# Kernel tuning notes

Hardware: AMD Instinct MI355X
Metric: run time of the kernel (lower is better)

The kernel has to match this reference:

```python
import jax, jax.numpy as jnp
import numpy as np

WINDOW_SIZE = 128
NEG = -1e9

def setup_inputs() -> dict:
    key = jax.random.key(0)
    kq, kk, kv = jax.random.split(key, 3)
    B, H, T, D = 2, 16, 2048, 64
    q = jax.random.normal(kq, (B, H, T, D), dtype=jnp.float32)
    k = jax.random.normal(kk, (B, H, T, D), dtype=jnp.float32)
    v = jax.random.normal(kv, (B, H, T, D), dtype=jnp.float32)
    return {"q": q, "k": k, "v": v}

def reference(q, k, v):
    # q,k,v: (B, H, T, D)
    D = q.shape[-1]
    Tq, Tk = q.shape[2], k.shape[2]
    scale = 1.0 / jnp.sqrt(jnp.asarray(D, dtype=q.dtype))
    scores = jnp.einsum('bhqd,bhkd->bhqk', q, k) * scale  # (B,H,Tq,Tk)
    dist = jnp.abs(jnp.arange(Tq)[:, None] - jnp.arange(Tk)[None, :])
    window_mask = dist <= WINDOW_SIZE  # (Tq,Tk)
    scores = jnp.where(window_mask[None, None], scores, jnp.asarray(NEG, dtype=scores.dtype))
    attn = jax.nn.softmax(scores, axis=-1)
    output = jnp.einsum('bhqk,bhkd->bhqd', attn, v)
    return (output, attn)
```

## Files before the change

kernel.cpp:

```cpp
#include <hip/hip_runtime.h>
#include <hip/hip_bf16.h>

typedef short bf16x8 __attribute__((ext_vector_type(8)));
typedef float f32x4 __attribute__((ext_vector_type(4)));

#define T_DIM 2048
#define D_DIM 64
#define WIN 128
#define QBLK 64
#define NEGBIG -1e30f
#define NZE 116

__device__ __forceinline__ short f2b(float x) {
  __hip_bfloat16 h = __float2bfloat16(x);
  return *reinterpret_cast<short*>(&h);
}
__device__ __forceinline__ float b2f(short s) {
  unsigned u = ((unsigned)(unsigned short)s) << 16;
  return __builtin_bit_cast(float, u);
}
__device__ __forceinline__ bf16x8 cvt8(f32x4 a, f32x4 b) {
  bf16x8 r;
  r[0] = f2b(a[0]); r[1] = f2b(a[1]); r[2] = f2b(a[2]); r[3] = f2b(a[3]);
  r[4] = f2b(b[0]); r[5] = f2b(b[1]); r[6] = f2b(b[2]); r[7] = f2b(b[3]);
  return r;
}
__device__ __forceinline__ int swzV(int row, int b) { return row * 640 + (b ^ ((row & 7) << 4)); }

#define ZEMIT(n) do { \
  for (int _i = 0; _i < (n); ++_i) { \
    if (zt < NZE) { \
      const int zr = (tid >> 3) + 32 * (zt & 1); \
      const int zc = (tid & 7) + 8 * (zt >> 1); \
      if (zc < rowg) { \
        const int c4 = zc << 2; \
        const int col = (c4 < Lw) ? c4 : (kend + c4 - Lw); \
        __builtin_nontemporal_store(zvec, (f32x4*)(azero + (size_t)zr * T_DIM + col)); \
      } \
      ++zt; \
    } \
  } } while (0)

__global__ __launch_bounds__(256, 3) void lsa_one(
    const float* __restrict__ Qg, const float* __restrict__ Kg,
    const float* __restrict__ Vg, float* __restrict__ Og,
    float* __restrict__ Ag) {
  const int tid = threadIdx.x;
  const int work = ((blockIdx.x & 7) << 7) + (blockIdx.x >> 3);
  const int bh = work >> 5;
  const int qb = work & 31;
  const int q0 = qb * QBLK;
  int kstart = q0 - WIN; if (kstart < 0) kstart = 0;
  int kend = q0 + QBLK + WIN; if (kend > T_DIM) kend = T_DIM;
  const int KW = kend - kstart;
  const int nkt = KW >> 4;
  const int ns = KW >> 5;
  const int Lw = kstart;
  const int rowg = (Lw + (T_DIM - kend)) >> 2;

  const float* qptr = Qg + (size_t)bh * (T_DIM * D_DIM);
  const float* kptr = Kg + (size_t)bh * (T_DIM * D_DIM);
  const float* vptr = Vg + (size_t)bh * (T_DIM * D_DIM);
  float* optr = Og + (size_t)bh * (T_DIM * D_DIM);
  float* aptr = Ag + (size_t)bh * ((size_t)T_DIM * T_DIM);
  float* azero = aptr + (size_t)q0 * T_DIM;

  __shared__ __align__(16) char Vb[D_DIM * 640];
  __shared__ __align__(16) char Pb[4 * 1024];

  for (int idx = tid; idx < KW * 16; idx += 256) {
    const int r = idx >> 4, c4 = idx & 15;
    f32x4 f = *(const f32x4*)(vptr + (size_t)(kstart + r) * D_DIM + c4 * 4);
    const int d0 = c4 * 4;
    *(short*)(Vb + swzV(d0 + 0, r * 2)) = f2b(f[0]);
    *(short*)(Vb + swzV(d0 + 1, r * 2)) = f2b(f[1]);
    *(short*)(Vb + swzV(d0 + 2, r * 2)) = f2b(f[2]);
    *(short*)(Vb + swzV(d0 + 3, r * 2)) = f2b(f[3]);
  }
  __syncthreads();

  const int lane = tid & 63, w = tid >> 6, c = lane & 15, hi = lane >> 4;
  const f32x4 zvec = {0.f, 0.f, 0.f, 0.f};
  int zt = 0;

  const float* qrow = qptr + (size_t)(q0 + w * 16 + c) * D_DIM + 8 * hi;
  const bf16x8 a0 = cvt8(*(const f32x4*)qrow, *(const f32x4*)(qrow + 4));
  const bf16x8 a1 = cvt8(*(const f32x4*)(qrow + 32), *(const f32x4*)(qrow + 36));

  int klo = q0 + w * 16 - WIN - kstart; if (klo < 0) klo = 0;
  const int kt0 = klo >> 4;
  int kt1 = (q0 + w * 16 + 15 + WIN + 1 - kstart + 15) >> 4; if (kt1 > nkt) kt1 = nkt;

  float m[4] = {NEGBIG, NEGBIG, NEGBIG, NEGBIG};
  float l[4] = {0.f, 0.f, 0.f, 0.f};
  for (int kt = kt0; kt < kt1; ++kt) {
    const float* krow = kptr + (size_t)(kstart + kt * 16 + c) * D_DIM + 8 * hi;
    const bf16x8 b0 = cvt8(*(const f32x4*)krow, *(const f32x4*)(krow + 4));
    const bf16x8 b1 = cvt8(*(const f32x4*)(krow + 32), *(const f32x4*)(krow + 36));
    f32x4 acc = {0.f, 0.f, 0.f, 0.f};
    acc = __builtin_amdgcn_mfma_f32_16x16x32_bf16(a0, b0, acc, 0, 0, 0);
    acc = __builtin_amdgcn_mfma_f32_16x16x32_bf16(a1, b1, acc, 0, 0, 0);
    const int kcol = kstart + kt * 16 + c;
#pragma unroll
    for (int j = 0; j < 4; ++j) {
      const int qr = q0 + w * 16 + 4 * hi + j;
      float s = acc[j] * 0.125f;
      int dist = qr - kcol; dist = dist < 0 ? -dist : dist;
      s = (dist <= WIN) ? s : NEGBIG;
      const float mn = fmaxf(m[j], s);
      l[j] = l[j] * __expf(m[j] - mn) + __expf(s - mn);
      m[j] = mn;
    }
    ZEMIT(4);
  }
#pragma unroll
  for (int j = 0; j < 4; ++j) {
#pragma unroll
    for (int d = 1; d <= 8; d <<= 1) {
      const float mo = __shfl_xor(m[j], d);
      const float lo = __shfl_xor(l[j], d);
      const float mn = fmaxf(m[j], mo);
      l[j] = l[j] * __expf(m[j] - mn) + lo * __expf(mo - mn);
      m[j] = mn;
    }
  }
  float il[4];
#pragma unroll
  for (int j = 0; j < 4; ++j) il[j] = 1.0f / l[j];

  char* pw = Pb + w * 1024;
  float* arow = aptr + (size_t)(q0 + w * 16 + c) * T_DIM + kstart;
  const int s0 = kt0 >> 1, s1 = (kt1 + 1) >> 1;

  f32x4 ov[4];
#pragma unroll
  for (int dt = 0; dt < 4; ++dt) ov[dt] = zvec;

  for (int s = 0; s < ns; ++s) {
    float* dst = arow + 32 * s + 8 * hi;
    if (s < s0 || s >= s1) {
      __builtin_nontemporal_store(zvec, (f32x4*)dst);
      __builtin_nontemporal_store(zvec, (f32x4*)(dst + 4));
      ZEMIT(5);
      continue;
    }
#pragma unroll
    for (int h = 0; h < 2; ++h) {
      const int kt = 2 * s + h;
      const float* krow = kptr + (size_t)(kstart + kt * 16 + c) * D_DIM + 8 * hi;
      const bf16x8 b0 = cvt8(*(const f32x4*)krow, *(const f32x4*)(krow + 4));
      const bf16x8 b1 = cvt8(*(const f32x4*)(krow + 32), *(const f32x4*)(krow + 36));
      f32x4 acc = {0.f, 0.f, 0.f, 0.f};
      acc = __builtin_amdgcn_mfma_f32_16x16x32_bf16(a0, b0, acc, 0, 0, 0);
      acc = __builtin_amdgcn_mfma_f32_16x16x32_bf16(a1, b1, acc, 0, 0, 0);
      const int kcol = kstart + kt * 16 + c;
#pragma unroll
      for (int j = 0; j < 4; ++j) {
        const int qr = q0 + w * 16 + 4 * hi + j;
        int dist = qr - kcol; dist = dist < 0 ? -dist : dist;
        const float p = (dist <= WIN) ? __expf(acc[j] * 0.125f - m[j]) * il[j] : 0.f;
        *(short*)(pw + (4 * hi + j) * 64 + ((2 * c + 32 * h) ^ (j << 4))) = f2b(p);
      }
    }
    const bf16x8 pa = *(const bf16x8*)(pw + c * 64 + ((16 * hi) ^ ((c & 3) << 4)));
    f32x4 o1, o2;
    o1[0] = b2f(pa[0]); o1[1] = b2f(pa[1]); o1[2] = b2f(pa[2]); o1[3] = b2f(pa[3]);
    o2[0] = b2f(pa[4]); o2[1] = b2f(pa[5]); o2[2] = b2f(pa[6]); o2[3] = b2f(pa[7]);
    __builtin_nontemporal_store(o1, (f32x4*)dst);
    __builtin_nontemporal_store(o2, (f32x4*)(dst + 4));
#pragma unroll
    for (int dt = 0; dt < 4; ++dt) {
      const bf16x8 vb = *(const bf16x8*)(Vb + swzV(dt * 16 + c, 64 * s + 16 * hi));
      ov[dt] = __builtin_amdgcn_mfma_f32_16x16x32_bf16(pa, vb, ov[dt], 0, 0, 0);
    }
    ZEMIT(5);
  }
  while (zt < NZE) ZEMIT(1);

#pragma unroll
  for (int dt = 0; dt < 4; ++dt)
#pragma unroll
    for (int j = 0; j < 4; ++j)
      __builtin_nontemporal_store(
          ov[dt][j], optr + (size_t)(q0 + w * 16 + 4 * hi + j) * D_DIM + dt * 16 + c);
}

extern "C" void kernel_launch(void* const* d_in, const int* in_sizes, int n_in,
                              void* d_out, int out_size, void* d_ws, size_t ws_size,
                              hipStream_t stream) {
  const float* q = (const float*)d_in[0];
  const float* k = (const float*)d_in[1];
  const float* v = (const float*)d_in[2];
  float* out = (float*)d_out;
  float* attn = out + (size_t)2 * 16 * T_DIM * D_DIM;
  lsa_one<<<dim3(2 * 16 * (T_DIM / QBLK)), dim3(256), 0, stream>>>(q, k, v, out, attn);
}
```

Baseline: 156.8 us.

## Warp-specialize zero-fill of attention matrix and software-prefetch K tiles

The block grows to 512 threads. The extra four waves only write the out-of-window zeros of the attention matrix, while the original four waves do the QK/softmax/PV compute; before, the compute waves interleaved those zero stores with their work. K rows are now loaded one tile ahead in both passes so global load latency overlaps the MFMA and exp work. The online-softmax update is rewritten to need one exp per element instead of two. The costs are more threads per block, which changes occupancy limits, and higher register pressure from the prefetch buffers.

```diff
diff --git a/kernel.cpp b/kernel.cpp
--- a/kernel.cpp
+++ b/kernel.cpp
@@ -9,7 +9,6 @@
 #define WIN 128
 #define QBLK 64
 #define NEGBIG -1e30f
-#define NZE 116
 
 __device__ __forceinline__ short f2b(float x) {
   __hip_bfloat16 h = __float2bfloat16(x);
@@ -27,48 +26,32 @@
 }
 __device__ __forceinline__ int swzV(int row, int b) { return row * 640 + (b ^ ((row & 7) << 4)); }
 
-#define ZEMIT(n) do { \
-  for (int _i = 0; _i < (n); ++_i) { \
-    if (zt < NZE) { \
-      const int zr = (tid >> 3) + 32 * (zt & 1); \
-      const int zc = (tid & 7) + 8 * (zt >> 1); \
-      if (zc < rowg) { \
-        const int c4 = zc << 2; \
-        const int col = (c4 < Lw) ? c4 : (kend + c4 - Lw); \
-        __builtin_nontemporal_store(zvec, (f32x4*)(azero + (size_t)zr * T_DIM + col)); \
-      } \
-      ++zt; \
-    } \
-  } } while (0)
-
-__global__ __launch_bounds__(256, 3) void lsa_one(
+#define KADDR(kt) (kptr + (size_t)(kstart + (kt) * 16 + c) * D_DIM + 8 * hi)
+#define LD4(kr, d0, d1, d2, d3) do { \
+  d0 = *(const f32x4*)(kr); d1 = *(const f32x4*)((kr) + 4); \
+  d2 = *(const f32x4*)((kr) + 32); d3 = *(const f32x4*)((kr) + 36); } while (0)
+
+__global__ __launch_bounds__(512, 4) void lsa_one(
     const float* __restrict__ Qg, const float* __restrict__ Kg,
     const float* __restrict__ Vg, float* __restrict__ Og,
     float* __restrict__ Ag) {
   const int tid = threadIdx.x;
   const int work = ((blockIdx.x & 7) << 7) + (blockIdx.x >> 3);
   const int bh = work >> 5;
-  const int qb = work & 31;
-  const int q0 = qb * QBLK;
+  const int q0 = (work & 31) * QBLK;
   int kstart = q0 - WIN; if (kstart < 0) kstart = 0;
   int kend = q0 + QBLK + WIN; if (kend > T_DIM) kend = T_DIM;
   const int KW = kend - kstart;
   const int nkt = KW >> 4;
   const int ns = KW >> 5;
-  const int Lw = kstart;
-  const int rowg = (Lw + (T_DIM - kend)) >> 2;
-
-  const float* qptr = Qg + (size_t)bh * (T_DIM * D_DIM);
-  const float* kptr = Kg + (size_t)bh * (T_DIM * D_DIM);
+
   const float* vptr = Vg + (size_t)bh * (T_DIM * D_DIM);
-  float* optr = Og + (size_t)bh * (T_DIM * D_DIM);
   float* aptr = Ag + (size_t)bh * ((size_t)T_DIM * T_DIM);
-  float* azero = aptr + (size_t)q0 * T_DIM;
 
   __shared__ __align__(16) char Vb[D_DIM * 640];
   __shared__ __align__(16) char Pb[4 * 1024];
 
-  for (int idx = tid; idx < KW * 16; idx += 256) {
+  for (int idx = tid; idx < KW * 16; idx += 512) {
     const int r = idx >> 4, c4 = idx & 15;
     f32x4 f = *(const f32x4*)(vptr + (size_t)(kstart + r) * D_DIM + c4 * 4);
     const int d0 = c4 * 4;
@@ -79,9 +62,25 @@
   }
   __syncthreads();
 
+  if (tid >= 256) {
+    const int t2 = tid - 256;
+    const int Lw = kstart;
+    const int zn = Lw + (T_DIM - kend);
+    const f32x4 z = {0.f, 0.f, 0.f, 0.f};
+    float* arow = aptr + (size_t)q0 * T_DIM;
+    for (int r = 0; r < QBLK; ++r, arow += T_DIM) {
+      for (int cc = t2 * 4; cc < zn; cc += 1024) {
+        const int col = (cc < Lw) ? cc : (kend + cc - Lw);
+        __builtin_nontemporal_store(z, (f32x4*)(arow + col));
+      }
+    }
+    return;
+  }
+
   const int lane = tid & 63, w = tid >> 6, c = lane & 15, hi = lane >> 4;
-  const f32x4 zvec = {0.f, 0.f, 0.f, 0.f};
-  int zt = 0;
+  const float* qptr = Qg + (size_t)bh * (T_DIM * D_DIM);
+  const float* kptr = Kg + (size_t)bh * (T_DIM * D_DIM);
+  float* optr = Og + (size_t)bh * (T_DIM * D_DIM);
 
   const float* qrow = qptr + (size_t)(q0 + w * 16 + c) * D_DIM + 8 * hi;
   const bf16x8 a0 = cvt8(*(const f32x4*)qrow, *(const f32x4*)(qrow + 4));
@@ -90,13 +89,16 @@
   int klo = q0 + w * 16 - WIN - kstart; if (klo < 0) klo = 0;
   const int kt0 = klo >> 4;
   int kt1 = (q0 + w * 16 + 15 + WIN + 1 - kstart + 15) >> 4; if (kt1 > nkt) kt1 = nkt;
-
+  const int s0 = kt0 >> 1, s1 = (kt1 + 1) >> 1;
+
+  f32x4 p0, p1, p2, p3;
+  { const float* kr = KADDR(kt0); LD4(kr, p0, p1, p2, p3); }
   float m[4] = {NEGBIG, NEGBIG, NEGBIG, NEGBIG};
   float l[4] = {0.f, 0.f, 0.f, 0.f};
   for (int kt = kt0; kt < kt1; ++kt) {
-    const float* krow = kptr + (size_t)(kstart + kt * 16 + c) * D_DIM + 8 * hi;
-    const bf16x8 b0 = cvt8(*(const f32x4*)krow, *(const f32x4*)(krow + 4));
-    const bf16x8 b1 = cvt8(*(const f32x4*)(krow + 32), *(const f32x4*)(krow + 36));
+    f32x4 n0 = p0, n1 = p1, n2 = p2, n3 = p3;
+    if (kt + 1 < kt1) { const float* kr = KADDR(kt + 1); LD4(kr, n0, n1, n2, n3); }
+    const bf16x8 b0 = cvt8(p0, p1), b1 = cvt8(p2, p3);
     f32x4 acc = {0.f, 0.f, 0.f, 0.f};
     acc = __builtin_amdgcn_mfma_f32_16x16x32_bf16(a0, b0, acc, 0, 0, 0);
     acc = __builtin_amdgcn_mfma_f32_16x16x32_bf16(a1, b1, acc, 0, 0, 0);
@@ -108,11 +110,15 @@
       int dist = qr - kcol; dist = dist < 0 ? -dist : dist;
       s = (dist <= WIN) ? s : NEGBIG;
       const float mn = fmaxf(m[j], s);
-      l[j] = l[j] * __expf(m[j] - mn) + __expf(s - mn);
+      const float e = __expf(fminf(s - m[j], m[j] - s));
+      l[j] = (s > m[j]) ? (l[j] * e + 1.f) : (l[j] + e);
       m[j] = mn;
     }
-    ZEMIT(4);
-  }
+    p0 = n0; p1 = n1; p2 = n2; p3 = n3;
+  }
+
+  { const float* kr = KADDR(2 * s0); LD4(kr, p0, p1, p2, p3); }
+
 #pragma unroll
   for (int j = 0; j < 4; ++j) {
 #pragma unroll
@@ -130,52 +136,55 @@
 
   char* pw = Pb + w * 1024;
   float* arow = aptr + (size_t)(q0 + w * 16 + c) * T_DIM + kstart;
-  const int s0 = kt0 >> 1, s1 = (kt1 + 1) >> 1;
-
+  const f32x4 zv = {0.f, 0.f, 0.f, 0.f};
   f32x4 ov[4];
 #pragma unroll
-  for (int dt = 0; dt < 4; ++dt) ov[dt] = zvec;
-
-  for (int s = 0; s < ns; ++s) {
+  for (int dt = 0; dt < 4; ++dt) ov[dt] = zv;
+
+  for (int kt = 2 * s0; kt < 2 * s1; ++kt) {
+    f32x4 n0 = p0, n1 = p1, n2 = p2, n3 = p3;
+    if (kt + 1 < 2 * s1) { const float* kr = KADDR(kt + 1); LD4(kr, n0, n1, n2, n3); }
+    const bf16x8 b0 = cvt8(p0, p1), b1 = cvt8(p2, p3);
+    f32x4 acc = {0.f, 0.f, 0.f, 0.f};
+    acc = __builtin_amdgcn_mfma_f32_16x16x32_bf16(a0, b0, acc, 0, 0, 0);
+    acc = __builtin_amdgcn_mfma_f32_16x16x32_bf16(a1, b1, acc, 0, 0, 0);
+    const int kcol = kstart + kt * 16 + c;
+    const int hb = (kt & 1) * 32;
+#pragma unroll
+    for (int j = 0; j < 4; ++j) {
+      const int qr = q0 + w * 16 + 4 * hi + j;
+      int dist = qr - kcol; dist = dist < 0 ? -dist : dist;
+      const float p = (dist <= WIN) ? __expf(acc[j] * 0.125f - m[j]) * il[j] : 0.f;
+      *(short*)(pw + (4 * hi + j) * 64 + ((2 * c + hb) ^ (j << 4))) = f2b(p);
+    }
+    if (kt & 1) {
+      const int s = kt >> 1;
+      const bf16x8 pa = *(const bf16x8*)(pw + c * 64 + ((16 * hi) ^ ((c & 3) << 4)));
+      f32x4 o1, o2;
+      o1[0] = b2f(pa[0]); o1[1] = b2f(pa[1]); o1[2] = b2f(pa[2]); o1[3] = b2f(pa[3]);
+      o2[0] = b2f(pa[4]); o2[1] = b2f(pa[5]); o2[2] = b2f(pa[6]); o2[3] = b2f(pa[7]);
+      float* dst = arow + 32 * s + 8 * hi;
+      __builtin_nontemporal_store(o1, (f32x4*)dst);
+      __builtin_nontemporal_store(o2, (f32x4*)(dst + 4));
+#pragma unroll
+      for (int dt = 0; dt < 4; ++dt) {
+        const bf16x8 vb = *(const bf16x8*)(Vb + swzV(dt * 16 + c, 64 * s + 16 * hi));
+        ov[dt] = __builtin_amdgcn_mfma_f32_16x16x32_bf16(pa, vb, ov[dt], 0, 0, 0);
+      }
+    }
+    p0 = n0; p1 = n1; p2 = n2; p3 = n3;
+  }
+
+  for (int s = 0; s < s0; ++s) {
     float* dst = arow + 32 * s + 8 * hi;
-    if (s < s0 || s >= s1) {
-      __builtin_nontemporal_store(zvec, (f32x4*)dst);
-      __builtin_nontemporal_store(zvec, (f32x4*)(dst + 4));
-      ZEMIT(5);
-      continue;
-    }
-#pragma unroll
-    for (int h = 0; h < 2; ++h) {
-      const int kt = 2 * s + h;
-      const float* krow = kptr + (size_t)(kstart + kt * 16 + c) * D_DIM + 8 * hi;
-      const bf16x8 b0 = cvt8(*(const f32x4*)krow, *(const f32x4*)(krow + 4));
-      const bf16x8 b1 = cvt8(*(const f32x4*)(krow + 32), *(const f32x4*)(krow + 36));
-      f32x4 acc = {0.f, 0.f, 0.f, 0.f};
-      acc = __builtin_amdgcn_mfma_f32_16x16x32_bf16(a0, b0, acc, 0, 0, 0);
-      acc = __builtin_amdgcn_mfma_f32_16x16x32_bf16(a1, b1, acc, 0, 0, 0);
-      const int kcol = kstart + kt * 16 + c;
-#pragma unroll
-      for (int j = 0; j < 4; ++j) {
-        const int qr = q0 + w * 16 + 4 * hi + j;
-        int dist = qr - kcol; dist = dist < 0 ? -dist : dist;
-        const float p = (dist <= WIN) ? __expf(acc[j] * 0.125f - m[j]) * il[j] : 0.f;
-        *(short*)(pw + (4 * hi + j) * 64 + ((2 * c + 32 * h) ^ (j << 4))) = f2b(p);
-      }
-    }
-    const bf16x8 pa = *(const bf16x8*)(pw + c * 64 + ((16 * hi) ^ ((c & 3) << 4)));
-    f32x4 o1, o2;
-    o1[0] = b2f(pa[0]); o1[1] = b2f(pa[1]); o1[2] = b2f(pa[2]); o1[3] = b2f(pa[3]);
-    o2[0] = b2f(pa[4]); o2[1] = b2f(pa[5]); o2[2] = b2f(pa[6]); o2[3] = b2f(pa[7]);
-    __builtin_nontemporal_store(o1, (f32x4*)dst);
-    __builtin_nontemporal_store(o2, (f32x4*)(dst + 4));
-#pragma unroll
-    for (int dt = 0; dt < 4; ++dt) {
-      const bf16x8 vb = *(const bf16x8*)(Vb + swzV(dt * 16 + c, 64 * s + 16 * hi));
-      ov[dt] = __builtin_amdgcn_mfma_f32_16x16x32_bf16(pa, vb, ov[dt], 0, 0, 0);
-    }
-    ZEMIT(5);
-  }
-  while (zt < NZE) ZEMIT(1);
+    __builtin_nontemporal_store(zv, (f32x4*)dst);
+    __builtin_nontemporal_store(zv, (f32x4*)(dst + 4));
+  }
+  for (int s = s1; s < ns; ++s) {
+    float* dst = arow + 32 * s + 8 * hi;
+    __builtin_nontemporal_store(zv, (f32x4*)dst);
+    __builtin_nontemporal_store(zv, (f32x4*)(dst + 4));
+  }
 
 #pragma unroll
   for (int dt = 0; dt < 4; ++dt)
@@ -193,5 +202,5 @@
   const float* v = (const float*)d_in[2];
   float* out = (float*)d_out;
   float* attn = out + (size_t)2 * 16 * T_DIM * D_DIM;
-  lsa_one<<<dim3(2 * 16 * (T_DIM / QBLK)), dim3(256), 0, stream>>>(q, k, v, out, attn);
-}
+  lsa_one<<<dim3(2 * 16 * (T_DIM / QBLK)), dim3(512), 0, stream>>>(q, k, v, out, attn);
+}
```

New measurement: 159.4 us. No clear change (+1.7%).
